# Kernel optimization log

Hardware: AMD Instinct MI355X
Metric: run time of the kernel (lower is better)

Reference implementation:

```python
import jax, jax.numpy as jnp
import numpy as np

TOP_K = 4


def setup_inputs() -> dict:
    key = jax.random.key(0)
    ks = jax.random.split(key, 6)
    B, S, H, I, E = 2, 1024, 1024, 1024, 16
    SD = I * 1  # shared_dim = moe_intermediate_size * n_shared_experts
    s = 0.02
    return {
        "hidden_states": jax.random.normal(ks[0], (B, S, H), jnp.float32),
        "gate_w": jax.random.normal(ks[1], (E, H), jnp.float32) * s,
        "w1": jax.random.normal(ks[2], (E, I, H), jnp.float32) * s,
        "w2": jax.random.normal(ks[3], (E, H, I), jnp.float32) * s,
        "shared_gu": jax.random.normal(ks[4], (2 * SD, H), jnp.float32) * s,
        "shared_down": jax.random.normal(ks[5], (H, SD), jnp.float32) * s,
    }


def reference(hidden_states, gate_w, w1, w2, shared_gu, shared_down):
    orig_shape = hidden_states.shape
    H = orig_shape[-1]
    x = hidden_states.reshape(-1, H)            # [T, H]
    T = x.shape[0]
    E = gate_w.shape[0]

    # --- router: softmax -> top-k -> renormalize ---
    logits = x @ gate_w.T                       # [T, E]
    probs = jax.nn.softmax(logits, axis=-1)
    topv, topi = jax.lax.top_k(probs, TOP_K)    # [T, K]
    topv = topv / jnp.sum(topv, axis=-1, keepdims=True)
    # dense routing-weight matrix [T, E] (zero for unselected experts)
    W = jnp.zeros((T, E), x.dtype).at[jnp.arange(T)[:, None], topi].set(topv)

    # --- routed experts: silu(x @ w1[e].T) @ w2[e].T, weighted ---
    h = jax.nn.silu(jnp.einsum('th,eih->tei', x, w1))      # [T, E, I]
    routed = jnp.einsum('tei,ehi,te->th', h, w2, W)        # [T, H]

    # --- shared expert SwiGLU ---
    gu = x @ shared_gu.T                        # [T, 2*SD]
    gate, up = jnp.split(gu, 2, axis=-1)
    shared = (jax.nn.silu(gate) * up) @ shared_down.T      # [T, H]

    return (routed + shared).reshape(orig_shape)
```

## Files before the change

### kernel.cpp

```cpp
#include <hip/hip_runtime.h>
#include <hip/hip_bf16.h>
#include <math.h>

using bf16 = __hip_bfloat16;

typedef __attribute__((ext_vector_type(4))) float fv4;
typedef __attribute__((ext_vector_type(4))) short sh4;
typedef __attribute__((ext_vector_type(8))) short sh8;
typedef __attribute__((ext_vector_type(4))) float f4acc;

#define T_TOK 2048
#define HD    1024
#define NE    16
#define KD    1024
#define NPAIR 8192

static constexpr size_t OFF_XB    = 0;
static constexpr size_t OFF_GUB   = 4194304;
static constexpr size_t OFF_ACT   = 12582912;
static constexpr size_t OFF_H1    = 16777216;
static constexpr size_t OFF_TOPI  = 33554432;
static constexpr size_t OFF_TOPV  = 33587200;
static constexpr size_t OFF_PTOK  = 33619968;
static constexpr size_t OFF_PWT   = 33652736;
static constexpr size_t OFF_OFFS  = 33685504;
static constexpr size_t OFF_CNT   = 33686016;
static constexpr size_t OFF_CBASE = 33686528;

__device__ __forceinline__ short f2bf(float f) {
  __hip_bfloat16 h = __float2bfloat16(f);
  union { __hip_bfloat16 b; short s; } u; u.b = h; return u.s;
}
__device__ __forceinline__ float bf2f(short s) {
  union { unsigned u; float f; } c; c.u = ((unsigned)(unsigned short)s) << 16; return c.f;
}
__device__ __forceinline__ void async16(const void* g, void* l) {
  __builtin_amdgcn_global_load_lds(
      (const __attribute__((address_space(1))) void*)g,
      (__attribute__((address_space(3))) void*)l, 16, 0, 0);
}

__global__ __launch_bounds__(256) void router_kernel(const float* __restrict__ x,
                                                     const float* __restrict__ gw,
                                                     int* __restrict__ topi,
                                                     float* __restrict__ topv,
                                                     short* __restrict__ xb,
                                                     float* __restrict__ out) {
  __shared__ float gsh[NE * HD];
  const int tid = threadIdx.x;
  const int wave = tid >> 6;
  const int lane = tid & 63;
  const int t = blockIdx.x * 4 + wave;

#pragma unroll
  for (int r = 0; r < 16; ++r) {
    int idx = r * 256 + tid;
    ((fv4*)gsh)[idx] = ((const fv4*)gw)[idx];
  }

  const float* xr = x + (size_t)t * HD;
  fv4 xa[4];
#pragma unroll
  for (int q = 0; q < 4; ++q) xa[q] = *(const fv4*)(xr + q * 256 + lane * 4);

#pragma unroll
  for (int q = 0; q < 4; ++q) {
    sh4 o; o[0]=f2bf(xa[q][0]); o[1]=f2bf(xa[q][1]); o[2]=f2bf(xa[q][2]); o[3]=f2bf(xa[q][3]);
    *(sh4*)(xb + (size_t)t * HD + q * 256 + lane * 4) = o;
    *(fv4*)(out + (size_t)t * HD + q * 256 + lane * 4) = (fv4)(0.f);
  }

  __syncthreads();

  float p[NE];
#pragma unroll
  for (int e = 0; e < NE; ++e) {
    const float* g = gsh + e * HD;
    float a = 0.f;
#pragma unroll
    for (int q = 0; q < 4; ++q) {
      fv4 gv = *(const fv4*)(g + q * 256 + lane * 4);
      a += xa[q][0] * gv[0] + xa[q][1] * gv[1] + xa[q][2] * gv[2] + xa[q][3] * gv[3];
    }
    p[e] = a;
  }
#pragma unroll
  for (int off = 1; off < 64; off <<= 1) {
#pragma unroll
    for (int e = 0; e < NE; ++e) p[e] += __shfl_xor(p[e], off);
  }

  int sel_i[4]; float sel_v[4];
#pragma unroll
  for (int k = 0; k < 4; ++k) {
    float best = p[0]; int bi = 0;
#pragma unroll
    for (int e = 1; e < NE; ++e) {
      bool c = p[e] > best;
      best = c ? p[e] : best;
      bi   = c ? e : bi;
    }
    sel_i[k] = bi; sel_v[k] = best;
#pragma unroll
    for (int e = 0; e < NE; ++e) p[e] = (e == bi) ? -3.4e38f : p[e];
  }
  float m = sel_v[0];
  float e0 = expf(sel_v[0] - m), e1 = expf(sel_v[1] - m);
  float e2 = expf(sel_v[2] - m), e3 = expf(sel_v[3] - m);
  float inv = 1.f / (e0 + e1 + e2 + e3);

  if (lane == 0) {
    topi[t * 4 + 0] = sel_i[0]; topv[t * 4 + 0] = e0 * inv;
    topi[t * 4 + 1] = sel_i[1]; topv[t * 4 + 1] = e1 * inv;
    topi[t * 4 + 2] = sel_i[2]; topv[t * 4 + 2] = e2 * inv;
    topi[t * 4 + 3] = sel_i[3]; topv[t * 4 + 3] = e3 * inv;
  }
}

__global__ __launch_bounds__(1024) void count_kernel(const int* __restrict__ topi,
                                                     int* __restrict__ cnt) {
  const int b = blockIdx.x;
  const int wave = threadIdx.x >> 6;
  const int lane = threadIdx.x & 63;
  const int base = b * 1024;
  int c = 0;
#pragma unroll
  for (int i = 0; i < 16; ++i) {
    unsigned long long m = __ballot(topi[base + i * 64 + lane] == wave);
    c += __popcll(m);
  }
  if (lane == 0) cnt[b * NE + wave] = c;
}

__global__ void scan2_kernel(const int* __restrict__ cnt,
                             int* __restrict__ offsets,
                             int* __restrict__ cbase) {
  if (threadIdx.x == 0 && blockIdx.x == 0) {
    int acc = 0;
    for (int e = 0; e < NE; ++e) {
      offsets[e] = acc;
      for (int b = 0; b < 8; ++b) { cbase[b * NE + e] = acc; acc += cnt[b * NE + e]; }
    }
    offsets[NE] = acc;
  }
}

__global__ __launch_bounds__(1024) void compact_kernel(const int* __restrict__ topi,
                                                       const float* __restrict__ topv,
                                                       const int* __restrict__ cbase,
                                                       int* __restrict__ ptok,
                                                       float* __restrict__ pwt) {
  const int b = blockIdx.x;
  const int wave = threadIdx.x >> 6;
  const int lane = threadIdx.x & 63;
  const int base = b * 1024;
  int slot = cbase[b * NE + wave];
#pragma unroll
  for (int i = 0; i < 16; ++i) {
    const int p = base + i * 64 + lane;
    const bool match = (topi[p] == wave);
    unsigned long long m = __ballot(match);
    unsigned long long lt = (lane == 0) ? 0ull : ((~0ull) >> (64 - lane));
    int pre = __popcll(m & lt);
    if (match) { ptok[slot + pre] = p >> 2; pwt[slot + pre] = topv[p]; }
    slot += __popcll(m);
  }
}

__global__ __launch_bounds__(256) void act_kernel(const short* __restrict__ gub,
                                                  short* __restrict__ act) {
  int i = blockIdx.x * 256 + threadIdx.x;
  int t = i >> 8, g = i & 255;
  sh4 gs = *(const sh4*)(gub + (size_t)t * 2048 + g * 4);
  sh4 us = *(const sh4*)(gub + (size_t)t * 2048 + 1024 + g * 4);
  sh4 o;
#pragma unroll
  for (int q = 0; q < 4; ++q) {
    float gg = bf2f(gs[q]);
    float s = gg / (1.f + expf(-gg)) * bf2f(us[q]);
    o[q] = f2bf(s);
  }
  *(sh4*)(act + (size_t)t * 1024 + g * 4) = o;
}

template <int PHASE>
__global__ __launch_bounds__(256) void gemm_pair_kernel(
    const bf16* __restrict__ A_sh, const bf16* __restrict__ A_rt,
    const float* __restrict__ B_sh, const float* __restrict__ B_rt,
    void* __restrict__ O_sh, void* __restrict__ O_rt,
    const int* __restrict__ ptok, const float* __restrict__ pwt,
    const int* __restrict__ offsets) {
  __shared__ bf16 Ash[2][128][32];
  __shared__ bf16 Bsh[2][128][32];

  const int tid = threadIdx.x;
  const int lane = tid & 63;
  const int wave = tid >> 6;
  const int wm = wave >> 1, wn = wave & 1;

  const bool routed = (int)blockIdx.x < 2048;
  int mt, nt, seg_start = 0, count = 0;
  const bf16* Abase;
  const float* Bpanel;
  if (routed) {
    int bid = blockIdx.x;
    int e = bid & 15;
    int r = bid >> 4;
    mt = r >> 3; nt = r & 7;
    seg_start = offsets[e];
    count = offsets[e + 1] - seg_start;
    if (mt * 128 >= count) return;
    Abase = A_rt;
    Bpanel = B_rt + ((size_t)e << 20) + (size_t)(nt * 128) * KD;
  } else {
    int sb = blockIdx.x - 2048;
    constexpr int nwg = (PHASE == 0) ? 256 : 128;
    constexpr int cpx = nwg >> 3;
    int sw = (sb & 7) * cpx + (sb >> 3);
    nt = sw >> 4; mt = sw & 15;
    count = 1 << 30;
    Abase = A_sh;
    Bpanel = B_sh + (size_t)(nt * 128) * KD;
  }

  const bf16* arow[2];
#pragma unroll
  for (int r = 0; r < 2; ++r) {
    int rowloc = r * 64 + wave * 16 + (lane >> 2);
    int grow;
    if (routed) {
      int slot = seg_start + mt * 128 + rowloc;
      if (slot > NPAIR - 1) slot = NPAIR - 1;
      grow = (PHASE == 0) ? ptok[slot] : slot;
    } else {
      grow = mt * 128 + rowloc;
    }
    arow[r] = Abase + (size_t)grow * KD + (lane & 3) * 8;
  }

  const float* brow[4];
  int bwrow[4], bwcol[4];
#pragma unroll
  for (int r = 0; r < 4; ++r) {
    int idx = (r << 8) + tid;
    int row = idx >> 3, cg = idx & 7;
    brow[r] = Bpanel + (size_t)row * KD + (cg << 2);
    bwrow[r] = row; bwcol[r] = cg << 2;
  }

  f4acc acc[4][4];
#pragma unroll
  for (int i = 0; i < 4; ++i)
#pragma unroll
    for (int j = 0; j < 4; ++j) acc[i][j] = (f4acc)(0.f);

  {
    fv4 b0 = *(const fv4*)(brow[0]);
    fv4 b1 = *(const fv4*)(brow[1]);
    fv4 b2 = *(const fv4*)(brow[2]);
    fv4 b3 = *(const fv4*)(brow[3]);
    async16(arow[0], (void*)&Ash[0][wave * 16][0]);
    async16(arow[1], (void*)&Ash[0][64 + wave * 16][0]);
    sh4 p0; p0[0]=f2bf(b0[0]); p0[1]=f2bf(b0[1]); p0[2]=f2bf(b0[2]); p0[3]=f2bf(b0[3]);
    sh4 p1; p1[0]=f2bf(b1[0]); p1[1]=f2bf(b1[1]); p1[2]=f2bf(b1[2]); p1[3]=f2bf(b1[3]);
    sh4 p2; p2[0]=f2bf(b2[0]); p2[1]=f2bf(b2[1]); p2[2]=f2bf(b2[2]); p2[3]=f2bf(b2[3]);
    sh4 p3; p3[0]=f2bf(b3[0]); p3[1]=f2bf(b3[1]); p3[2]=f2bf(b3[2]); p3[3]=f2bf(b3[3]);
    *(sh4*)&Bsh[0][bwrow[0]][bwcol[0]] = p0;
    *(sh4*)&Bsh[0][bwrow[1]][bwcol[1]] = p1;
    *(sh4*)&Bsh[0][bwrow[2]][bwcol[2]] = p2;
    *(sh4*)&Bsh[0][bwrow[3]][bwcol[3]] = p3;
  }
  __syncthreads();

  int buf = 0;
  for (int kt = 0; kt < 32; ++kt) {
    const int k0n = (kt + 1) * 32;
    const bool has_next = (kt < 31);
    fv4 n0, n1, n2, n3;
    if (has_next) {
      async16(arow[0] + k0n, (void*)&Ash[buf ^ 1][wave * 16][0]);
      async16(arow[1] + k0n, (void*)&Ash[buf ^ 1][64 + wave * 16][0]);
      n0 = *(const fv4*)(brow[0] + k0n);
      n1 = *(const fv4*)(brow[1] + k0n);
      n2 = *(const fv4*)(brow[2] + k0n);
      n3 = *(const fv4*)(brow[3] + k0n);
    }

    sh8 fa[4], fb[4];
#pragma unroll
    for (int mi = 0; mi < 4; ++mi)
      fa[mi] = *(const sh8*)&Ash[buf][wm * 64 + mi * 16 + (lane & 15)][(lane >> 4) * 8];
#pragma unroll
    for (int ni = 0; ni < 4; ++ni)
      fb[ni] = *(const sh8*)&Bsh[buf][wn * 64 + ni * 16 + (lane & 15)][(lane >> 4) * 8];
#pragma unroll
    for (int mi = 0; mi < 4; ++mi)
#pragma unroll
      for (int ni = 0; ni < 4; ++ni)
        acc[mi][ni] = __builtin_amdgcn_mfma_f32_16x16x32_bf16(fa[mi], fb[ni], acc[mi][ni], 0, 0, 0);

    if (has_next) {
      sh4 p0; p0[0]=f2bf(n0[0]); p0[1]=f2bf(n0[1]); p0[2]=f2bf(n0[2]); p0[3]=f2bf(n0[3]);
      sh4 p1; p1[0]=f2bf(n1[0]); p1[1]=f2bf(n1[1]); p1[2]=f2bf(n1[2]); p1[3]=f2bf(n1[3]);
      sh4 p2; p2[0]=f2bf(n2[0]); p2[1]=f2bf(n2[1]); p2[2]=f2bf(n2[2]); p2[3]=f2bf(n2[3]);
      sh4 p3; p3[0]=f2bf(n3[0]); p3[1]=f2bf(n3[1]); p3[2]=f2bf(n3[2]); p3[3]=f2bf(n3[3]);
      *(sh4*)&Bsh[buf ^ 1][bwrow[0]][bwcol[0]] = p0;
      *(sh4*)&Bsh[buf ^ 1][bwrow[1]][bwcol[1]] = p1;
      *(sh4*)&Bsh[buf ^ 1][bwrow[2]][bwcol[2]] = p2;
      *(sh4*)&Bsh[buf ^ 1][bwrow[3]][bwcol[3]] = p3;
    }
    __syncthreads();
    buf ^= 1;
  }

  if (PHASE == 0) {
    if (routed) {
#pragma unroll
      for (int mi = 0; mi < 4; ++mi) {
#pragma unroll
        for (int j = 0; j < 4; ++j) {
          int rloc = wm * 64 + mi * 16 + (lane >> 4) * 4 + j;
          if (mt * 128 + rloc >= count) continue;
          size_t orow = (size_t)(seg_start + mt * 128 + rloc) * 1024 + nt * 128;
#pragma unroll
          for (int ni = 0; ni < 4; ++ni) {
            int cloc = wn * 64 + ni * 16 + (lane & 15);
            float v = acc[mi][ni][j];
            float s = v / (1.f + expf(-v));
            ((short*)O_rt)[orow + cloc] = f2bf(s);
          }
        }
      }
    } else {
#pragma unroll
      for (int mi = 0; mi < 4; ++mi) {
#pragma unroll
        for (int j = 0; j < 4; ++j) {
          int rloc = wm * 64 + mi * 16 + (lane >> 4) * 4 + j;
          size_t orow = (size_t)(mt * 128 + rloc) * 2048 + nt * 128;
#pragma unroll
          for (int ni = 0; ni < 4; ++ni) {
            int cloc = wn * 64 + ni * 16 + (lane & 15);
            ((short*)O_sh)[orow + cloc] = f2bf(acc[mi][ni][j]);
          }
        }
      }
    }
  } else {
    if (routed) {
#pragma unroll
      for (int mi = 0; mi < 4; ++mi) {
#pragma unroll
        for (int j = 0; j < 4; ++j) {
          int rloc = wm * 64 + mi * 16 + (lane >> 4) * 4 + j;
          if (mt * 128 + rloc >= count) continue;
          int slot = seg_start + mt * 128 + rloc;
          int token = ptok[slot];
          float w = pwt[slot];
          float* orow = (float*)O_rt + (size_t)token * 1024 + nt * 128;
#pragma unroll
          for (int ni = 0; ni < 4; ++ni) {
            int cloc = wn * 64 + ni * 16 + (lane & 15);
            unsafeAtomicAdd(orow + cloc, w * acc[mi][ni][j]);
          }
        }
      }
    } else {
#pragma unroll
      for (int mi = 0; mi < 4; ++mi) {
#pragma unroll
        for (int j = 0; j < 4; ++j) {
          int rloc = wm * 64 + mi * 16 + (lane >> 4) * 4 + j;
          float* orow = (float*)O_sh + (size_t)(mt * 128 + rloc) * 1024 + nt * 128;
#pragma unroll
          for (int ni = 0; ni < 4; ++ni) {
            int cloc = wn * 64 + ni * 16 + (lane & 15);
            unsafeAtomicAdd(orow + cloc, acc[mi][ni][j]);
          }
        }
      }
    }
  }
}

extern "C" void kernel_launch(void* const* d_in, const int* in_sizes, int n_in,
                              void* d_out, int out_size, void* d_ws, size_t ws_size,
                              hipStream_t stream) {
  const float* x   = (const float*)d_in[0];
  const float* gw  = (const float*)d_in[1];
  const float* w1  = (const float*)d_in[2];
  const float* w2  = (const float*)d_in[3];
  const float* sgu = (const float*)d_in[4];
  const float* sdn = (const float*)d_in[5];
  float* out = (float*)d_out;

  char* ws = (char*)d_ws;
  bf16*  xb    = (bf16*)(ws + OFF_XB);
  bf16*  gub   = (bf16*)(ws + OFF_GUB);
  bf16*  act   = (bf16*)(ws + OFF_ACT);
  bf16*  h1    = (bf16*)(ws + OFF_H1);
  int*   topi  = (int*)(ws + OFF_TOPI);
  float* topv  = (float*)(ws + OFF_TOPV);
  int*   ptok  = (int*)(ws + OFF_PTOK);
  float* pwt   = (float*)(ws + OFF_PWT);
  int*   offs  = (int*)(ws + OFF_OFFS);
  int*   cnt   = (int*)(ws + OFF_CNT);
  int*   cbase = (int*)(ws + OFF_CBASE);

  router_kernel<<<512, 256, 0, stream>>>(x, gw, topi, topv, (short*)xb, out);
  count_kernel<<<8, 1024, 0, stream>>>(topi, cnt);
  scan2_kernel<<<1, 64, 0, stream>>>(cnt, offs, cbase);
  compact_kernel<<<8, 1024, 0, stream>>>(topi, topv, cbase, ptok, pwt);

  gemm_pair_kernel<0><<<2304, 256, 0, stream>>>(xb, xb, sgu, w1,
                                                gub, h1, ptok, pwt, offs);
  act_kernel<<<2048, 256, 0, stream>>>((const short*)gub, (short*)act);

  gemm_pair_kernel<1><<<2176, 256, 0, stream>>>(act, h1, sdn, w2,
                                                out, out, ptok, pwt, offs);
}
```

Measured before the change: 165.1 us.

## Pre-convert down-proj weights to bf16 inside first GEMM, async-load in second

The first grouped GEMM kernel now also converts w2 and the shared down-projection weights from fp32 to bf16 into workspace. It does this at the start of every block, including routed blocks that exit early. The second GEMM then reads bf16 weights through async global-to-LDS loads instead of loading fp32 and converting in registers. This halves B-operand traffic in the second GEMM and simplifies its pipeline. The cost is an extra full read and write of the weights (~70MB) inside the first kernel, which adds memory traffic that may outweigh the savings.

```diff
diff --git a/kernel.cpp b/kernel.cpp
--- a/kernel.cpp
+++ b/kernel.cpp
@@ -19,13 +19,15 @@
 static constexpr size_t OFF_GUB   = 4194304;
 static constexpr size_t OFF_ACT   = 12582912;
 static constexpr size_t OFF_H1    = 16777216;
-static constexpr size_t OFF_TOPI  = 33554432;
-static constexpr size_t OFF_TOPV  = 33587200;
-static constexpr size_t OFF_PTOK  = 33619968;
-static constexpr size_t OFF_PWT   = 33652736;
-static constexpr size_t OFF_OFFS  = 33685504;
-static constexpr size_t OFF_CNT   = 33686016;
-static constexpr size_t OFF_CBASE = 33686528;
+static constexpr size_t OFF_W2B   = 33554432;
+static constexpr size_t OFF_SDNB  = 67108864;
+static constexpr size_t OFF_TOPI  = 69206016;
+static constexpr size_t OFF_TOPV  = 69238784;
+static constexpr size_t OFF_PTOK  = 69271552;
+static constexpr size_t OFF_PWT   = 69304320;
+static constexpr size_t OFF_OFFS  = 69337088;
+static constexpr size_t OFF_CNT   = 69337600;
+static constexpr size_t OFF_CBASE = 69338112;
 
 __device__ __forceinline__ short f2bf(float f) {
   __hip_bfloat16 h = __float2bfloat16(f);
@@ -183,10 +185,11 @@
   *(sh4*)(act + (size_t)t * 1024 + g * 4) = o;
 }
 
-template <int PHASE>
-__global__ __launch_bounds__(256) void gemm_pair_kernel(
+__global__ __launch_bounds__(256) void gemm_k2_kernel(
     const bf16* __restrict__ A_sh, const bf16* __restrict__ A_rt,
     const float* __restrict__ B_sh, const float* __restrict__ B_rt,
+    const float* __restrict__ w2, const float* __restrict__ sdn,
+    short* __restrict__ w2b, short* __restrict__ sdnb,
     void* __restrict__ O_sh, void* __restrict__ O_rt,
     const int* __restrict__ ptok, const float* __restrict__ pwt,
     const int* __restrict__ offsets) {
@@ -197,6 +200,24 @@
   const int lane = tid & 63;
   const int wave = tid >> 6;
   const int wm = wave >> 1, wn = wave & 1;
+
+  if ((int)blockIdx.x < 2048) {
+    const size_t base = (size_t)blockIdx.x * 2048 + tid;
+#pragma unroll
+    for (int it = 0; it < 8; ++it) {
+      fv4 v = ((const fv4*)w2)[base + it * 256];
+      sh4 o; o[0]=f2bf(v[0]); o[1]=f2bf(v[1]); o[2]=f2bf(v[2]); o[3]=f2bf(v[3]);
+      ((sh4*)w2b)[base + it * 256] = o;
+    }
+  } else {
+    const size_t base = (size_t)(blockIdx.x - 2048) * 1024 + tid;
+#pragma unroll
+    for (int it = 0; it < 4; ++it) {
+      fv4 v = ((const fv4*)sdn)[base + it * 256];
+      sh4 o; o[0]=f2bf(v[0]); o[1]=f2bf(v[1]); o[2]=f2bf(v[2]); o[3]=f2bf(v[3]);
+      ((sh4*)sdnb)[base + it * 256] = o;
+    }
+  }
 
   const bool routed = (int)blockIdx.x < 2048;
   int mt, nt, seg_start = 0, count = 0;
@@ -214,8 +235,7 @@
     Bpanel = B_rt + ((size_t)e << 20) + (size_t)(nt * 128) * KD;
   } else {
     int sb = blockIdx.x - 2048;
-    constexpr int nwg = (PHASE == 0) ? 256 : 128;
-    constexpr int cpx = nwg >> 3;
+    constexpr int cpx = 256 >> 3;
     int sw = (sb & 7) * cpx + (sb >> 3);
     nt = sw >> 4; mt = sw & 15;
     count = 1 << 30;
@@ -231,7 +251,7 @@
     if (routed) {
       int slot = seg_start + mt * 128 + rowloc;
       if (slot > NPAIR - 1) slot = NPAIR - 1;
-      grow = (PHASE == 0) ? ptok[slot] : slot;
+      grow = ptok[slot];
     } else {
       grow = mt * 128 + rowloc;
     }
@@ -313,70 +333,163 @@
     buf ^= 1;
   }
 
-  if (PHASE == 0) {
-    if (routed) {
-#pragma unroll
-      for (int mi = 0; mi < 4; ++mi) {
-#pragma unroll
-        for (int j = 0; j < 4; ++j) {
-          int rloc = wm * 64 + mi * 16 + (lane >> 4) * 4 + j;
-          if (mt * 128 + rloc >= count) continue;
-          size_t orow = (size_t)(seg_start + mt * 128 + rloc) * 1024 + nt * 128;
-#pragma unroll
-          for (int ni = 0; ni < 4; ++ni) {
-            int cloc = wn * 64 + ni * 16 + (lane & 15);
-            float v = acc[mi][ni][j];
-            float s = v / (1.f + expf(-v));
-            ((short*)O_rt)[orow + cloc] = f2bf(s);
-          }
+  if (routed) {
+#pragma unroll
+    for (int mi = 0; mi < 4; ++mi) {
+#pragma unroll
+      for (int j = 0; j < 4; ++j) {
+        int rloc = wm * 64 + mi * 16 + (lane >> 4) * 4 + j;
+        if (mt * 128 + rloc >= count) continue;
+        size_t orow = (size_t)(seg_start + mt * 128 + rloc) * 1024 + nt * 128;
+#pragma unroll
+        for (int ni = 0; ni < 4; ++ni) {
+          int cloc = wn * 64 + ni * 16 + (lane & 15);
+          float v = acc[mi][ni][j];
+          float s = v / (1.f + expf(-v));
+          ((short*)O_rt)[orow + cloc] = f2bf(s);
         }
       }
-    } else {
-#pragma unroll
-      for (int mi = 0; mi < 4; ++mi) {
-#pragma unroll
-        for (int j = 0; j < 4; ++j) {
-          int rloc = wm * 64 + mi * 16 + (lane >> 4) * 4 + j;
-          size_t orow = (size_t)(mt * 128 + rloc) * 2048 + nt * 128;
-#pragma unroll
-          for (int ni = 0; ni < 4; ++ni) {
-            int cloc = wn * 64 + ni * 16 + (lane & 15);
-            ((short*)O_sh)[orow + cloc] = f2bf(acc[mi][ni][j]);
-          }
+    }
+  } else {
+#pragma unroll
+    for (int mi = 0; mi < 4; ++mi) {
+#pragma unroll
+      for (int j = 0; j < 4; ++j) {
+        int rloc = wm * 64 + mi * 16 + (lane >> 4) * 4 + j;
+        size_t orow = (size_t)(mt * 128 + rloc) * 2048 + nt * 128;
+#pragma unroll
+        for (int ni = 0; ni < 4; ++ni) {
+          int cloc = wn * 64 + ni * 16 + (lane & 15);
+          ((short*)O_sh)[orow + cloc] = f2bf(acc[mi][ni][j]);
         }
       }
     }
+  }
+}
+
+__global__ __launch_bounds__(256) void gemm_k3_kernel(
+    const bf16* __restrict__ A_sh, const bf16* __restrict__ A_rt,
+    const bf16* __restrict__ B_sh, const bf16* __restrict__ B_rt,
+    float* __restrict__ out,
+    const int* __restrict__ ptok, const float* __restrict__ pwt,
+    const int* __restrict__ offsets) {
+  __shared__ bf16 Ash[2][128][32];
+  __shared__ bf16 Bsh[2][128][32];
+
+  const int tid = threadIdx.x;
+  const int lane = tid & 63;
+  const int wave = tid >> 6;
+  const int wm = wave >> 1, wn = wave & 1;
+
+  const bool routed = (int)blockIdx.x < 2048;
+  int mt, nt, seg_start = 0, count = 0;
+  const bf16* Abase;
+  const bf16* Bpanel;
+  if (routed) {
+    int bid = blockIdx.x;
+    int e = bid & 15;
+    int r = bid >> 4;
+    mt = r >> 3; nt = r & 7;
+    seg_start = offsets[e];
+    count = offsets[e + 1] - seg_start;
+    if (mt * 128 >= count) return;
+    Abase = A_rt;
+    Bpanel = B_rt + ((size_t)e << 20) + (size_t)(nt * 128) * KD;
   } else {
+    int sb = blockIdx.x - 2048;
+    constexpr int cpx = 128 >> 3;
+    int sw = (sb & 7) * cpx + (sb >> 3);
+    nt = sw >> 4; mt = sw & 15;
+    count = 1 << 30;
+    Abase = A_sh;
+    Bpanel = B_sh + (size_t)(nt * 128) * KD;
+  }
+
+  const bf16* arow[2];
+  const bf16* brow[2];
+#pragma unroll
+  for (int r = 0; r < 2; ++r) {
+    int rowloc = r * 64 + wave * 16 + (lane >> 2);
+    int grow;
     if (routed) {
-#pragma unroll
-      for (int mi = 0; mi < 4; ++mi) {
-#pragma unroll
-        for (int j = 0; j < 4; ++j) {
-          int rloc = wm * 64 + mi * 16 + (lane >> 4) * 4 + j;
-          if (mt * 128 + rloc >= count) continue;
-          int slot = seg_start + mt * 128 + rloc;
-          int token = ptok[slot];
-          float w = pwt[slot];
-          float* orow = (float*)O_rt + (size_t)token * 1024 + nt * 128;
-#pragma unroll
-          for (int ni = 0; ni < 4; ++ni) {
-            int cloc = wn * 64 + ni * 16 + (lane & 15);
-            unsafeAtomicAdd(orow + cloc, w * acc[mi][ni][j]);
-          }
+      int slot = seg_start + mt * 128 + rowloc;
+      if (slot > NPAIR - 1) slot = NPAIR - 1;
+      grow = slot;
+    } else {
+      grow = mt * 128 + rowloc;
+    }
+    arow[r] = Abase + (size_t)grow * KD + (lane & 3) * 8;
+    brow[r] = Bpanel + (size_t)rowloc * KD + (lane & 3) * 8;
+  }
+
+  f4acc acc[4][4];
+#pragma unroll
+  for (int i = 0; i < 4; ++i)
+#pragma unroll
+    for (int j = 0; j < 4; ++j) acc[i][j] = (f4acc)(0.f);
+
+  async16(arow[0], (void*)&Ash[0][wave * 16][0]);
+  async16(arow[1], (void*)&Ash[0][64 + wave * 16][0]);
+  async16(brow[0], (void*)&Bsh[0][wave * 16][0]);
+  async16(brow[1], (void*)&Bsh[0][64 + wave * 16][0]);
+  __syncthreads();
+
+  int buf = 0;
+  for (int kt = 0; kt < 32; ++kt) {
+    const int k0n = (kt + 1) * 32;
+    if (kt < 31) {
+      async16(arow[0] + k0n, (void*)&Ash[buf ^ 1][wave * 16][0]);
+      async16(arow[1] + k0n, (void*)&Ash[buf ^ 1][64 + wave * 16][0]);
+      async16(brow[0] + k0n, (void*)&Bsh[buf ^ 1][wave * 16][0]);
+      async16(brow[1] + k0n, (void*)&Bsh[buf ^ 1][64 + wave * 16][0]);
+    }
+
+    sh8 fa[4], fb[4];
+#pragma unroll
+    for (int mi = 0; mi < 4; ++mi)
+      fa[mi] = *(const sh8*)&Ash[buf][wm * 64 + mi * 16 + (lane & 15)][(lane >> 4) * 8];
+#pragma unroll
+    for (int ni = 0; ni < 4; ++ni)
+      fb[ni] = *(const sh8*)&Bsh[buf][wn * 64 + ni * 16 + (lane & 15)][(lane >> 4) * 8];
+#pragma unroll
+    for (int mi = 0; mi < 4; ++mi)
+#pragma unroll
+      for (int ni = 0; ni < 4; ++ni)
+        acc[mi][ni] = __builtin_amdgcn_mfma_f32_16x16x32_bf16(fa[mi], fb[ni], acc[mi][ni], 0, 0, 0);
+
+    __syncthreads();
+    buf ^= 1;
+  }
+
+  if (routed) {
+#pragma unroll
+    for (int mi = 0; mi < 4; ++mi) {
+#pragma unroll
+      for (int j = 0; j < 4; ++j) {
+        int rloc = wm * 64 + mi * 16 + (lane >> 4) * 4 + j;
+        if (mt * 128 + rloc >= count) continue;
+        int slot = seg_start + mt * 128 + rloc;
+        int token = ptok[slot];
+        float w = pwt[slot];
+        float* orow = out + (size_t)token * 1024 + nt * 128;
+#pragma unroll
+        for (int ni = 0; ni < 4; ++ni) {
+          int cloc = wn * 64 + ni * 16 + (lane & 15);
+          unsafeAtomicAdd(orow + cloc, w * acc[mi][ni][j]);
         }
       }
-    } else {
-#pragma unroll
-      for (int mi = 0; mi < 4; ++mi) {
-#pragma unroll
-        for (int j = 0; j < 4; ++j) {
-          int rloc = wm * 64 + mi * 16 + (lane >> 4) * 4 + j;
-          float* orow = (float*)O_sh + (size_t)(mt * 128 + rloc) * 1024 + nt * 128;
-#pragma unroll
-          for (int ni = 0; ni < 4; ++ni) {
-            int cloc = wn * 64 + ni * 16 + (lane & 15);
-            unsafeAtomicAdd(orow + cloc, acc[mi][ni][j]);
-          }
+    }
+  } else {
+#pragma unroll
+    for (int mi = 0; mi < 4; ++mi) {
+#pragma unroll
+      for (int j = 0; j < 4; ++j) {
+        int rloc = wm * 64 + mi * 16 + (lane >> 4) * 4 + j;
+        float* orow = out + (size_t)(mt * 128 + rloc) * 1024 + nt * 128;
+#pragma unroll
+        for (int ni = 0; ni < 4; ++ni) {
+          int cloc = wn * 64 + ni * 16 + (lane & 15);
+          unsafeAtomicAdd(orow + cloc, acc[mi][ni][j]);
         }
       }
     }
@@ -399,6 +512,8 @@
   bf16*  gub   = (bf16*)(ws + OFF_GUB);
   bf16*  act   = (bf16*)(ws + OFF_ACT);
   bf16*  h1    = (bf16*)(ws + OFF_H1);
+  bf16*  w2b   = (bf16*)(ws + OFF_W2B);
+  bf16*  sdnb  = (bf16*)(ws + OFF_SDNB);
   int*   topi  = (int*)(ws + OFF_TOPI);
   float* topv  = (float*)(ws + OFF_TOPV);
   int*   ptok  = (int*)(ws + OFF_PTOK);
@@ -412,10 +527,11 @@
   scan2_kernel<<<1, 64, 0, stream>>>(cnt, offs, cbase);
   compact_kernel<<<8, 1024, 0, stream>>>(topi, topv, cbase, ptok, pwt);
 
-  gemm_pair_kernel<0><<<2304, 256, 0, stream>>>(xb, xb, sgu, w1,
-                                                gub, h1, ptok, pwt, offs);
+  gemm_k2_kernel<<<2304, 256, 0, stream>>>(xb, xb, sgu, w1, w2, sdn,
+                                           (short*)w2b, (short*)sdnb,
+                                           gub, h1, ptok, pwt, offs);
   act_kernel<<<2048, 256, 0, stream>>>((const short*)gub, (short*)act);
 
-  gemm_pair_kernel<1><<<2176, 256, 0, stream>>>(act, h1, sdn, w2,
-                                                out, out, ptok, pwt, offs);
-}
+  gemm_k3_kernel<<<2176, 256, 0, stream>>>(act, h1, sdnb, w2b,
+                                           out, ptok, pwt, offs);
+}
```

Result: no change. 165.9 us (+0.5%).
